# Kernel optimization log

Hardware: AMD Instinct MI355X
Metric: run time of the kernel (lower is better)

The kernel has to match this reference:

```python
import jax, jax.numpy as jnp
import numpy as np

B, S, HID = 1, 8192, 768
H, D = 12, 64          # num heads, head dim (HID = H*D)
W = 256                # one-sided attention window


def _shift_chunks(xc, C):
    # xc: [B, C, w, H, D] -> prev/next chunk copies padded with zeros
    prev = jnp.pad(xc, ((0, 0), (1, 0), (0, 0), (0, 0), (0, 0)))[:, :C]
    nxt = jnp.pad(xc, ((0, 0), (0, 1), (0, 0), (0, 0), (0, 0)))[:, 1:]
    return jnp.concatenate([prev, xc, nxt], axis=2)  # [B, C, 3w, H, D]


def sliding_window_attention(q, k, v, w):
    # q,k,v: [B, S, H, D]; q already scaled. Band width 2w+1.
    b, s, h, d = q.shape
    c = s // w
    qc = q.reshape(b, c, w, h, d)
    k3 = _shift_chunks(k.reshape(b, c, w, h, d), c)  # [b,c,3w,h,d]
    v3 = _shift_chunks(v.reshape(b, c, w, h, d), c)
    # scores of each query chunk against its 3-chunk key neighborhood
    scores3 = jnp.einsum('bcxhd,bcyhd->bhcxy', qc, k3)  # [b,h,c,w,3w]
    rows = jnp.arange(w)
    offs = jnp.arange(2 * w + 1)
    gidx = rows[:, None] + offs[None, :]  # [w, 2w+1] local key index p+j
    band = scores3[..., rows[:, None], gidx]  # [b,h,c,w,2w+1]
    # mask keys outside [0, S) (same effect as mask_invalid_locations)
    gq = jnp.arange(s).reshape(c, w)                    # global query pos
    keypos = gq[..., None] + (offs - w)                 # [c,w,2w+1]
    valid = (keypos >= 0) & (keypos < s)
    band = jnp.where(valid[None, None], band, -jnp.inf)
    prob = jax.nn.softmax(band, axis=-1)
    prob = jnp.where(valid[None, None], prob, 0.0)
    # scatter band probs back to 3w layout, then banded PV matmul
    prob3 = jnp.zeros(band.shape[:-1] + (3 * w,), band.dtype)
    prob3 = prob3.at[..., rows[:, None], gidx].set(prob)  # [b,h,c,w,3w]
    ctx = jnp.einsum('bhcxy,bcyhd->bcxhd', prob3, v3)
    return ctx.reshape(b, s, h, d)


def setup_inputs() -> dict:
    key = jax.random.key(0)
    ks = jax.random.split(key, 4)
    sc = 1.0 / np.sqrt(HID)
    return {
        'hidden_states': jax.random.normal(ks[0], (B, S, HID), jnp.float32),
        'Wq': jax.random.normal(ks[1], (HID, HID), jnp.float32) * sc,
        'bq': jnp.zeros((HID,), jnp.float32),
        'Wk': jax.random.normal(ks[2], (HID, HID), jnp.float32) * sc,
        'bk': jnp.zeros((HID,), jnp.float32),
        'Wv': jax.random.normal(ks[3], (HID, HID), jnp.float32) * sc,
        'bv': jnp.zeros((HID,), jnp.float32),
    }


def reference(hidden_states, Wq, bq, Wk, bk, Wv, bv):
    b, s, hid = hidden_states.shape
    q = (hidden_states @ Wq + bq).reshape(b, s, H, D)
    k = (hidden_states @ Wk + bk).reshape(b, s, H, D)
    v = (hidden_states @ Wv + bv).reshape(b, s, H, D)
    q = q / jnp.asarray(np.sqrt(D), q.dtype)
    ctx = sliding_window_attention(q, k, v, W)  # [b,s,H,D]
    return ctx.reshape(b, s, hid)
```

## Files before the change

### kernel.cpp

```cpp
#include <hip/hip_runtime.h>
#include <hip/hip_bf16.h>

#define S_LEN 8192
#define HID 768
#define NH 12
#define HD 64
#define WIN 256

typedef __bf16 bf16x8 __attribute__((ext_vector_type(8)));
typedef float f32x4 __attribute__((ext_vector_type(4)));
using bf16_t = __hip_bfloat16;

#define MFMA(a, b, c) __builtin_amdgcn_mfma_f32_16x16x32_bf16(a, b, c, 0, 0, 0)

__device__ __forceinline__ void gl2lds16(const bf16_t* g, bf16_t* l) {
  __builtin_amdgcn_global_load_lds(
      (const __attribute__((address_space(1))) void*)g,
      (__attribute__((address_space(3))) void*)l, 16, 0, 0);
}

__global__ __launch_bounds__(256) void conv_hs(const float* __restrict__ hs,
                                               bf16_t* __restrict__ hb) {
  int i = (blockIdx.x * 256 + threadIdx.x) * 4;
  float4 v = *reinterpret_cast<const float4*>(hs + i);
  union { ushort4 u; bf16_t b[4]; } H;
  H.b[0] = __float2bfloat16(v.x);
  H.b[1] = __float2bfloat16(v.y);
  H.b[2] = __float2bfloat16(v.z);
  H.b[3] = __float2bfloat16(v.w);
  *reinterpret_cast<ushort4*>(hb + i) = H.u;
}

__global__ __launch_bounds__(256) void transpose_w(const float* __restrict__ Wq,
                                                   const float* __restrict__ Wk,
                                                   const float* __restrict__ Wv,
                                                   bf16_t* __restrict__ Wt) {
  __shared__ float t[32][33];
  int z = blockIdx.z;
  const float* src = (z == 0) ? Wq : ((z == 1) ? Wk : Wv);
  int n0 = blockIdx.x * 32, k0 = blockIdx.y * 32;
  int tx = threadIdx.x, ty = threadIdx.y;
  for (int i = 0; i < 4; ++i)
    t[ty + i * 8][tx] = src[(k0 + ty + i * 8) * HID + n0 + tx];
  __syncthreads();
  bf16_t* dst = Wt + z * HID * HID;
  for (int i = 0; i < 4; ++i)
    dst[(n0 + ty + i * 8) * HID + k0 + tx] = __float2bfloat16(t[tx][ty + i * 8]);
}

__global__ __launch_bounds__(256) void qkv_gemm(
    const bf16_t* __restrict__ hb, const bf16_t* __restrict__ Wt,
    const float* __restrict__ bq, const float* __restrict__ bk,
    const float* __restrict__ bv,
    bf16_t* __restrict__ Qw, bf16_t* __restrict__ Kw, bf16_t* __restrict__ Vt) {
  __shared__ __align__(16) bf16_t sA[128 * 64];
  __shared__ __align__(16) bf16_t sB[128 * 64];
  int m0 = blockIdx.x * 128;
  int zq = blockIdx.y / 6;
  int nn0 = (blockIdx.y % 6) * 128;
  int n0g = zq * HID + nn0;
  int tid = threadIdx.x;
  int w = tid >> 6, lane = tid & 63, lm = lane & 15, qd = lane >> 4;
  int wm = w & 1, wn = w >> 1;

  int srow = w * 8 + (lane >> 3);
  int sc8 = (lane & 7) ^ ((lane >> 3) & 7);
  const bf16_t* gA = hb + (m0 + srow) * HID + sc8 * 8;
  const bf16_t* gB = Wt + (n0g + srow) * HID + sc8 * 8;
  int sx0 = lm & 7;

  f32x4 acc[4][4] = {};
  for (int kk = 0; kk < HID; kk += 64) {
#pragma unroll
    for (int u = 0; u < 4; ++u) {
      gl2lds16(gA + (u * 32) * HID + kk, sA + u * 2048 + w * 512);
      gl2lds16(gB + (u * 32) * HID + kk, sB + u * 2048 + w * 512);
    }
    __syncthreads();
#pragma unroll
    for (int half = 0; half < 2; ++half) {
      int ca = (qd + 4 * half) ^ sx0;
      bf16x8 fa[4], fb[4];
#pragma unroll
      for (int i = 0; i < 4; ++i) {
        fa[i] = *reinterpret_cast<const bf16x8*>(
            sA + (wm * 64 + i * 16 + lm) * 64 + ca * 8);
        fb[i] = *reinterpret_cast<const bf16x8*>(
            sB + (wn * 64 + i * 16 + lm) * 64 + ca * 8);
      }
      if (zq == 2) {
#pragma unroll
        for (int i = 0; i < 4; ++i)
#pragma unroll
          for (int j = 0; j < 4; ++j)
            acc[i][j] = MFMA(fa[i], fb[j], acc[i][j]);
      } else {
#pragma unroll
        for (int i = 0; i < 4; ++i)
#pragma unroll
          for (int j = 0; j < 4; ++j)
            acc[i][j] = MFMA(fb[i], fa[j], acc[i][j]);
      }
    }
    __syncthreads();
  }

  if (zq != 2) {
    const float* bias = zq ? bk : bq;
    bf16_t* dst = zq ? Kw : Qw;
    float scale = zq ? 1.0f : 0.125f;
#pragma unroll
    for (int i = 0; i < 4; ++i) {
      int nbase = nn0 + wn * 64 + i * 16 + qd * 4;
      float4 b4 = *reinterpret_cast<const float4*>(bias + nbase);
      int h = nbase >> 6, d0 = nbase & 63;
#pragma unroll
      for (int j = 0; j < 4; ++j) {
        int m = m0 + wm * 64 + j * 16 + lm;
        union { ushort4 u; bf16_t b[4]; } P;
        P.b[0] = __float2bfloat16((acc[i][j][0] + b4.x) * scale);
        P.b[1] = __float2bfloat16((acc[i][j][1] + b4.y) * scale);
        P.b[2] = __float2bfloat16((acc[i][j][2] + b4.z) * scale);
        P.b[3] = __float2bfloat16((acc[i][j][3] + b4.w) * scale);
        *reinterpret_cast<ushort4*>(dst + (h * S_LEN + m) * HD + d0) = P.u;
      }
    }
  } else {
#pragma unroll
    for (int i = 0; i < 4; ++i) {
      int mb = m0 + wm * 64 + i * 16 + qd * 4;
#pragma unroll
      for (int j = 0; j < 4; ++j) {
        int nl = nn0 + wn * 64 + j * 16 + lm;
        float bb = bv[nl];
        union { ushort4 u; bf16_t b[4]; } P;
        P.b[0] = __float2bfloat16(acc[i][j][0] + bb);
        P.b[1] = __float2bfloat16(acc[i][j][1] + bb);
        P.b[2] = __float2bfloat16(acc[i][j][2] + bb);
        P.b[3] = __float2bfloat16(acc[i][j][3] + bb);
        *reinterpret_cast<ushort4*>(Vt + nl * S_LEN + mb) = P.u;
      }
    }
  }
}

__global__ __launch_bounds__(256) void swa_kernel(
    const bf16_t* __restrict__ Qw, const bf16_t* __restrict__ Kw,
    const bf16_t* __restrict__ Vt, float* __restrict__ out) {
  __shared__ __align__(16) bf16_t sK[2][64 * 64];
  __shared__ __align__(16) bf16_t sV[2][64 * 64];
  __shared__ __align__(16) bf16_t sP[4 * 16 * 72];
  int h = blockIdx.y;
  int nb = blockIdx.x;
  int q0 = (((nb & 7) << 4) | (nb >> 3)) * 64;
  int tid = threadIdx.x;
  int w = tid >> 6, lane = tid & 63, lm = lane & 15, qd = lane >> 4;
  int xb = q0 + w * 16;

  int qoff = (h * S_LEN + xb + lm) * HD + qd * 8;
  bf16x8 aq0 = *reinterpret_cast<const bf16x8*>(Qw + qoff);
  bf16x8 aq1 = *reinterpret_cast<const bf16x8*>(Qw + qoff + 32);

  f32x4 o[4] = {};
  float lsum = 0.f;

  int y_begin = q0 - WIN; if (y_begin < 0) y_begin = 0;
  int y_end = q0 + 64 + WIN; if (y_end > S_LEN) y_end = S_LEN;
  int ntiles = (y_end - y_begin) >> 6;
  const bf16_t* Kh = Kw + h * S_LEN * HD;
  const bf16_t* Vh = Vt + h * HD * S_LEN;
  bf16_t* sPw = sP + w * 16 * 72;

  int srow = w * 8 + (lane >> 3);
  int sc8 = (lane & 7) ^ ((lane >> 3) & 7);
  int sx0 = lm & 7;

#define STAGE(y0, b)                                                    \
  {                                                                     \
    const bf16_t* kg = Kh + ((y0) + srow) * HD + sc8 * 8;               \
    gl2lds16(kg, &sK[b][w * 512]);                                      \
    gl2lds16(kg + 32 * HD, &sK[b][2048 + w * 512]);                     \
    const bf16_t* vg = Vh + srow * S_LEN + (y0) + sc8 * 8;              \
    gl2lds16(vg, &sV[b][w * 512]);                                      \
    gl2lds16(vg + 32 * S_LEN, &sV[b][2048 + w * 512]);                  \
  }

  STAGE(y_begin, 0);
  __syncthreads();

  for (int t = 0; t < ntiles; ++t) {
    int y0 = y_begin + t * 64;
    if (t + 1 < ntiles) STAGE(y0 + 64, (t + 1) & 1);
    int b = t & 1;
    f32x4 s[4] = {};
#pragma unroll
    for (int nt = 0; nt < 4; ++nt) {
      const bf16_t* kr = &sK[b][(nt * 16 + lm) * 64];
      bf16x8 b0 = *reinterpret_cast<const bf16x8*>(kr + (qd ^ sx0) * 8);
      bf16x8 b1 = *reinterpret_cast<const bf16x8*>(kr + ((qd + 4) ^ sx0) * 8);
      s[nt] = MFMA(b0, aq0, s[nt]);
      s[nt] = MFMA(b1, aq1, s[nt]);
    }
    int dy = y0 - q0;
    bool edge = (dy > 192) || (dy < -192);
#pragma unroll
    for (int nt = 0; nt < 4; ++nt) {
      union { ushort4 u; bf16_t b[4]; } P;
#pragma unroll
      for (int r = 0; r < 4; ++r) {
        float pv;
        if (edge) {
          int dlt = (y0 + nt * 16 + qd * 4 + r) - (xb + lm);
          pv = (dlt <= WIN && dlt >= -WIN) ? __expf(s[nt][r]) : 0.f;
        } else {
          pv = __expf(s[nt][r]);
        }
        lsum += pv;
        P.b[r] = __float2bfloat16(pv);
      }
      *reinterpret_cast<ushort4*>(sPw + lm * 72 + nt * 16 + qd * 4) = P.u;
    }
    bf16x8 ap0 = *reinterpret_cast<const bf16x8*>(sPw + lm * 72 + qd * 8);
    bf16x8 ap1 = *reinterpret_cast<const bf16x8*>(sPw + lm * 72 + 32 + qd * 8);
#pragma unroll
    for (int nt = 0; nt < 4; ++nt) {
      const bf16_t* vr = &sV[b][(nt * 16 + lm) * 64];
      bf16x8 v0 = *reinterpret_cast<const bf16x8*>(vr + (qd ^ sx0) * 8);
      bf16x8 v1 = *reinterpret_cast<const bf16x8*>(vr + ((qd + 4) ^ sx0) * 8);
      o[nt] = MFMA(ap0, v0, o[nt]);
      o[nt] = MFMA(ap1, v1, o[nt]);
    }
    __syncthreads();
  }
  lsum += __shfl_xor(lsum, 16);
  lsum += __shfl_xor(lsum, 32);
#pragma unroll
  for (int r = 0; r < 4; ++r) {
    float inv = 1.f / __shfl(lsum, qd * 4 + r);
    int x = xb + qd * 4 + r;
#pragma unroll
    for (int nt = 0; nt < 4; ++nt)
      out[x * HID + h * HD + nt * 16 + lm] = o[nt][r] * inv;
  }
}

extern "C" void kernel_launch(void* const* d_in, const int* in_sizes, int n_in,
                              void* d_out, int out_size, void* d_ws, size_t ws_size,
                              hipStream_t stream) {
  const float* hs = (const float*)d_in[0];
  const float* Wq = (const float*)d_in[1];
  const float* bq = (const float*)d_in[2];
  const float* Wk = (const float*)d_in[3];
  const float* bk = (const float*)d_in[4];
  const float* Wv = (const float*)d_in[5];
  const float* bv = (const float*)d_in[6];
  float* out = (float*)d_out;

  const int NSH = S_LEN * HID;
  const int NW = 3 * HID * HID;
  bf16_t* p = (bf16_t*)d_ws;
  bf16_t* hb = p; p += NSH;
  bf16_t* Wt = p; p += NW;
  bf16_t* Qw = p; p += NSH;
  bf16_t* Kw = p; p += NSH;
  bf16_t* Vt = p; p += NSH;

  conv_hs<<<dim3(NSH / 4 / 256), dim3(256), 0, stream>>>(hs, hb);
  transpose_w<<<dim3(24, 24, 3), dim3(32, 8), 0, stream>>>(Wq, Wk, Wv, Wt);
  qkv_gemm<<<dim3(64, 18), dim3(256), 0, stream>>>(
      hb, Wt, bq, bk, bv, Qw, Kw, Vt);
  swa_kernel<<<dim3(128, 12), dim3(256), 0, stream>>>(Qw, Kw, Vt, out);
}
```

Before: 177.3 us.

## Process 128 queries per SWA block, reuse K/V tiles, skip out-of-band subtiles

Each attention block now covers 128 queries, with every wave handling two 16-row query subtiles. This halves the number of K/V tiles staged per query and reuses the K/V register fragments across both subtiles. Subtiles entirely outside the ±256 band skip their MFMAs, which removes wasted score and PV work at the tile edges. The change also pads the P scratch stride to 76 and halves the grid to 64x12 blocks. That lowers occupancy and parallelism and raises register pressure.

```diff
diff --git a/kernel.cpp b/kernel.cpp
--- a/kernel.cpp
+++ b/kernel.cpp
@@ -144,32 +144,36 @@
   }
 }
 
+#define PST 76
 __global__ __launch_bounds__(256) void swa_kernel(
     const bf16_t* __restrict__ Qw, const bf16_t* __restrict__ Kw,
     const bf16_t* __restrict__ Vt, float* __restrict__ out) {
   __shared__ __align__(16) bf16_t sK[2][64 * 64];
   __shared__ __align__(16) bf16_t sV[2][64 * 64];
-  __shared__ __align__(16) bf16_t sP[4 * 16 * 72];
+  __shared__ __align__(16) bf16_t sP[4 * 16 * PST];
   int h = blockIdx.y;
   int nb = blockIdx.x;
-  int q0 = (((nb & 7) << 4) | (nb >> 3)) * 64;
+  int q0 = (((nb & 7) << 3) | (nb >> 3)) * 128;
   int tid = threadIdx.x;
   int w = tid >> 6, lane = tid & 63, lm = lane & 15, qd = lane >> 4;
-  int xb = q0 + w * 16;
-
-  int qoff = (h * S_LEN + xb + lm) * HD + qd * 8;
-  bf16x8 aq0 = *reinterpret_cast<const bf16x8*>(Qw + qoff);
-  bf16x8 aq1 = *reinterpret_cast<const bf16x8*>(Qw + qoff + 32);
-
-  f32x4 o[4] = {};
-  float lsum = 0.f;
+
+  bf16x8 aq[2][2];
+#pragma unroll
+  for (int ss = 0; ss < 2; ++ss) {
+    int qoff = (h * S_LEN + q0 + w * 32 + ss * 16 + lm) * HD + qd * 8;
+    aq[ss][0] = *reinterpret_cast<const bf16x8*>(Qw + qoff);
+    aq[ss][1] = *reinterpret_cast<const bf16x8*>(Qw + qoff + 32);
+  }
+
+  f32x4 o[2][4] = {};
+  float lsum[2] = {0.f, 0.f};
 
   int y_begin = q0 - WIN; if (y_begin < 0) y_begin = 0;
-  int y_end = q0 + 64 + WIN; if (y_end > S_LEN) y_end = S_LEN;
+  int y_end = q0 + 128 + WIN; if (y_end > S_LEN) y_end = S_LEN;
   int ntiles = (y_end - y_begin) >> 6;
   const bf16_t* Kh = Kw + h * S_LEN * HD;
   const bf16_t* Vh = Vt + h * HD * S_LEN;
-  bf16_t* sPw = sP + w * 16 * 72;
+  bf16_t* sPw = sP + w * 16 * PST;
 
   int srow = w * 8 + (lane >> 3);
   int sc8 = (lane & 7) ^ ((lane >> 3) & 7);
@@ -192,55 +196,69 @@
     int y0 = y_begin + t * 64;
     if (t + 1 < ntiles) STAGE(y0 + 64, (t + 1) & 1);
     int b = t & 1;
-    f32x4 s[4] = {};
+    bf16x8 kf[4][2], vf[4][2];
 #pragma unroll
     for (int nt = 0; nt < 4; ++nt) {
       const bf16_t* kr = &sK[b][(nt * 16 + lm) * 64];
-      bf16x8 b0 = *reinterpret_cast<const bf16x8*>(kr + (qd ^ sx0) * 8);
-      bf16x8 b1 = *reinterpret_cast<const bf16x8*>(kr + ((qd + 4) ^ sx0) * 8);
-      s[nt] = MFMA(b0, aq0, s[nt]);
-      s[nt] = MFMA(b1, aq1, s[nt]);
-    }
-    int dy = y0 - q0;
-    bool edge = (dy > 192) || (dy < -192);
-#pragma unroll
-    for (int nt = 0; nt < 4; ++nt) {
-      union { ushort4 u; bf16_t b[4]; } P;
-#pragma unroll
-      for (int r = 0; r < 4; ++r) {
-        float pv;
-        if (edge) {
-          int dlt = (y0 + nt * 16 + qd * 4 + r) - (xb + lm);
-          pv = (dlt <= WIN && dlt >= -WIN) ? __expf(s[nt][r]) : 0.f;
-        } else {
-          pv = __expf(s[nt][r]);
+      kf[nt][0] = *reinterpret_cast<const bf16x8*>(kr + (qd ^ sx0) * 8);
+      kf[nt][1] = *reinterpret_cast<const bf16x8*>(kr + ((qd + 4) ^ sx0) * 8);
+      const bf16_t* vr = &sV[b][(nt * 16 + lm) * 64];
+      vf[nt][0] = *reinterpret_cast<const bf16x8*>(vr + (qd ^ sx0) * 8);
+      vf[nt][1] = *reinterpret_cast<const bf16x8*>(vr + ((qd + 4) ^ sx0) * 8);
+    }
+#pragma unroll
+    for (int ss = 0; ss < 2; ++ss) {
+      int qs = q0 + w * 32 + ss * 16;
+      int dy = y0 - qs;
+      if (dy < -319 || dy > 271) continue;
+      bool full = (dy >= -241) && (dy <= 193);
+      f32x4 s[4] = {};
+#pragma unroll
+      for (int nt = 0; nt < 4; ++nt) {
+        s[nt] = MFMA(kf[nt][0], aq[ss][0], s[nt]);
+        s[nt] = MFMA(kf[nt][1], aq[ss][1], s[nt]);
+      }
+#pragma unroll
+      for (int nt = 0; nt < 4; ++nt) {
+        union { ushort4 u; bf16_t b[4]; } P;
+#pragma unroll
+        for (int r = 0; r < 4; ++r) {
+          float pv;
+          if (full) {
+            pv = __expf(s[nt][r]);
+          } else {
+            int dlt = (y0 + nt * 16 + qd * 4 + r) - (qs + lm);
+            pv = (dlt <= WIN && dlt >= -WIN) ? __expf(s[nt][r]) : 0.f;
+          }
+          lsum[ss] += pv;
+          P.b[r] = __float2bfloat16(pv);
         }
-        lsum += pv;
-        P.b[r] = __float2bfloat16(pv);
-      }
-      *reinterpret_cast<ushort4*>(sPw + lm * 72 + nt * 16 + qd * 4) = P.u;
-    }
-    bf16x8 ap0 = *reinterpret_cast<const bf16x8*>(sPw + lm * 72 + qd * 8);
-    bf16x8 ap1 = *reinterpret_cast<const bf16x8*>(sPw + lm * 72 + 32 + qd * 8);
-#pragma unroll
-    for (int nt = 0; nt < 4; ++nt) {
-      const bf16_t* vr = &sV[b][(nt * 16 + lm) * 64];
-      bf16x8 v0 = *reinterpret_cast<const bf16x8*>(vr + (qd ^ sx0) * 8);
-      bf16x8 v1 = *reinterpret_cast<const bf16x8*>(vr + ((qd + 4) ^ sx0) * 8);
-      o[nt] = MFMA(ap0, v0, o[nt]);
-      o[nt] = MFMA(ap1, v1, o[nt]);
+        *reinterpret_cast<ushort4*>(sPw + lm * PST + nt * 16 + qd * 4) = P.u;
+      }
+      bf16x8 ap0 = *reinterpret_cast<const bf16x8*>(sPw + lm * PST + qd * 8);
+      bf16x8 ap1 = *reinterpret_cast<const bf16x8*>(sPw + lm * PST + 32 + qd * 8);
+#pragma unroll
+      for (int nt = 0; nt < 4; ++nt) {
+        o[ss][nt] = MFMA(ap0, vf[nt][0], o[ss][nt]);
+        o[ss][nt] = MFMA(ap1, vf[nt][1], o[ss][nt]);
+      }
     }
     __syncthreads();
   }
-  lsum += __shfl_xor(lsum, 16);
-  lsum += __shfl_xor(lsum, 32);
-#pragma unroll
-  for (int r = 0; r < 4; ++r) {
-    float inv = 1.f / __shfl(lsum, qd * 4 + r);
-    int x = xb + qd * 4 + r;
-#pragma unroll
-    for (int nt = 0; nt < 4; ++nt)
-      out[x * HID + h * HD + nt * 16 + lm] = o[nt][r] * inv;
+#pragma unroll
+  for (int ss = 0; ss < 2; ++ss) {
+    float v = lsum[ss];
+    v += __shfl_xor(v, 16);
+    v += __shfl_xor(v, 32);
+    int qs = q0 + w * 32 + ss * 16;
+#pragma unroll
+    for (int r = 0; r < 4; ++r) {
+      float inv = 1.f / __shfl(v, qd * 4 + r);
+      int x = qs + qd * 4 + r;
+#pragma unroll
+      for (int nt = 0; nt < 4; ++nt)
+        out[x * HID + h * HD + nt * 16 + lm] = o[ss][nt][r] * inv;
+    }
   }
 }
 
@@ -269,5 +287,5 @@
   transpose_w<<<dim3(24, 24, 3), dim3(32, 8), 0, stream>>>(Wq, Wk, Wv, Wt);
   qkv_gemm<<<dim3(64, 18), dim3(256), 0, stream>>>(
       hb, Wt, bq, bk, bv, Qw, Kw, Vt);
-  swa_kernel<<<dim3(128, 12), dim3(256), 0, stream>>>(Qw, Kw, Vt, out);
-}
+  swa_kernel<<<dim3(64, 12), dim3(256), 0, stream>>>(Qw, Kw, Vt, out);
+}
```

Measured after the change: 193.4 us. +9.1%, slower.
